# Optimization experiments

Measured on AMD Instinct MI355X. Metric: run time of the kernel, lower is better.

The kernel has to match this reference:

```python
import jax, jax.numpy as jnp
import numpy as np

MIN_SIZE = 16.0
PH, PW, SCALE = 7, 7, 0.0625


def _context_anchor(rois, hh, hw):
    """rois: [N,5] (batch_idx,x1,y1,x2,y2). Returns [N*8,5] context boxes, col0 = 0 label."""
    N = rois.shape[0]
    x1, y1, x2, y2 = rois[:, 1], rois[:, 2], rois[:, 3], rois[:, 4]
    w, h = x2 - x1, y2 - y1
    k = jnp.arange(3, dtype=rois.dtype)
    sx = x1[:, None] + w[:, None] * (k - 0.5)  # x1 - w + w*k + w/2
    sy = y1[:, None] + h[:, None] * (k - 0.5)
    # np.meshgrid(shift_x, shift_y).ravel() is y-major
    cx = jnp.broadcast_to(sx[:, None, :], (N, 3, 3)).reshape(N, 9)
    cy = jnp.broadcast_to(sy[:, :, None], (N, 3, 3)).reshape(N, 9)
    boxes = jnp.stack([cx - w[:, None] / 4, cy - h[:, None] / 4,
                       cx + w[:, None] / 4, cy + h[:, None] / 4], -1)  # [N,9,4]
    bw = boxes[..., 2] - boxes[..., 0] + 1
    bh = boxes[..., 3] - boxes[..., 1] + 1
    invalid = ((boxes[..., 0] < 0) | (boxes[..., 1] < 0) |
               (boxes[..., 2] >= hw) | (boxes[..., 3] >= hh) |
               (bw < MIN_SIZE) | (bh < MIN_SIZE))
    boxes = jnp.where(invalid[..., None], rois[:, None, 1:5], boxes)
    boxes = boxes[:, jnp.array([0, 1, 2, 3, 5, 6, 7, 8]), :]  # drop center cell
    gt = boxes.reshape(N * 8, 4)  # K = 8N
    # IoU(all roi boxes, gt) with +1 pixel convention (bbox_overlaps_batch)
    A = rois[:, 1:5]
    aw, ah = A[:, 2] - A[:, 0] + 1, A[:, 3] - A[:, 1] + 1
    gw, gh = gt[:, 2] - gt[:, 0] + 1, gt[:, 3] - gt[:, 1] + 1
    iw = jnp.maximum(jnp.minimum(A[:, None, 2], gt[None, :, 2]) - jnp.maximum(A[:, None, 0], gt[None, :, 0]) + 1, 0)
    ih = jnp.maximum(jnp.minimum(A[:, None, 3], gt[None, :, 3]) - jnp.maximum(A[:, None, 1], gt[None, :, 1]) + 1, 0)
    inter = iw * ih
    ov = inter / ((aw * ah)[:, None] + (gw * gh)[None, :] - inter)  # [N,K]
    ov = jnp.where(((gw == 1) & (gh == 1))[None, :], 0.0, ov)
    ov = jnp.where(((aw == 1) & (ah == 1))[:, None], -1.0, ov)
    gt_max = ov.max(0)          # best overlap per gt box
    best = ov.argmax(0)         # index of best-matching roi (torch's `_`)
    labels = gt_max >= 0.3
    w_cell, h_cell = gt[:, 2] - gt[:, 0], gt[:, 3] - gt[:, 1]
    rw = jnp.where(labels, rois[best, 3] - rois[best, 1], 0.0)
    rh = jnp.where(labels, rois[best, 4] - rois[best, 2], 0.0)
    labels = (labels & ~(jnp.maximum(rw, rh) >= jnp.maximum(w_cell, h_cell))
                     & ~(jnp.minimum(rw, rh) < jnp.minimum(w_cell, h_cell) / 3))
    gt = jnp.where(labels[:, None], rois[best][:, 1:5], gt)
    # original zeroes labels at the end -> label column is all zeros
    return jnp.concatenate([jnp.zeros((N * 8, 1), rois.dtype), gt], -1)


def _roi_pool(features, boxes, ph, pw, scale):
    """Classic Caffe max RoIPool. Assumes batch_size==1 (all batch indices 0)."""
    _, C, H, W = features.shape
    f = features[0]  # [C,H,W]
    sw = jnp.round(boxes[:, 1] * scale)
    sh = jnp.round(boxes[:, 2] * scale)
    ew = jnp.round(boxes[:, 3] * scale)
    eh = jnp.round(boxes[:, 4] * scale)
    bsh = jnp.maximum(eh - sh + 1, 1.0) / ph
    bsw = jnp.maximum(ew - sw + 1, 1.0) / pw
    ii = jnp.arange(ph, dtype=f.dtype)
    jj = jnp.arange(pw, dtype=f.dtype)
    hs = jnp.clip(jnp.floor(ii[None, :] * bsh[:, None]) + sh[:, None], 0, H)   # [R,ph]
    he = jnp.clip(jnp.ceil((ii[None, :] + 1) * bsh[:, None]) + sh[:, None], 0, H)
    ws = jnp.clip(jnp.floor(jj[None, :] * bsw[:, None]) + sw[:, None], 0, W)   # [R,pw]
    we = jnp.clip(jnp.ceil((jj[None, :] + 1) * bsw[:, None]) + sw[:, None], 0, W)
    hidx = jnp.arange(H, dtype=f.dtype)
    widx = jnp.arange(W, dtype=f.dtype)
    mask_h = (hidx >= hs[..., None]) & (hidx < he[..., None])  # [R,ph,H]
    mask_w = (widx >= ws[..., None]) & (widx < we[..., None])  # [R,pw,W]
    NEG = jnp.asarray(-1e30, f.dtype)
    # separable masked max: reduce W per pw-bin, then H per ph-bin
    colmax = jnp.stack([jnp.where(mask_w[:, j, None, None, :], f[None], NEG).max(-1)
                        for j in range(pw)], axis=1)           # [R,pw,C,H]
    out = jnp.stack([jnp.where(mask_h[:, i, None, None, :], colmax, NEG).max(-1)
                     for i in range(ph)], axis=1)              # [R,ph,pw,C]
    valid = mask_h.any(-1)[:, :, None] & mask_w.any(-1)[:, None, :]
    out = jnp.where(valid[..., None], out, 0.0)                # empty bins -> 0
    return jnp.transpose(out, (0, 3, 1, 2))                    # [R,C,ph,pw]


def reference(features, rois, hh, hw):
    N = rois.shape[0]
    gt = _context_anchor(rois, hh, hw).reshape(N, 8, 5)
    cat_rois = jnp.concatenate([rois[:, None, :], gt], 1).reshape(-1, 5)  # [9N,5]
    pool = _roi_pool(features, cat_rois, PH, PW, SCALE)                   # [9N,C,7,7]
    pool_feat = pool.reshape(N, -1, PW, PH)                               # [N,9C,7,7]
    return pool_feat, cat_rois


def setup_inputs() -> dict:
    key = jax.random.key(0)
    k1, k2, k3, k4, k5 = jax.random.split(key, 5)
    N, C, Hf, Wf, IMG = 32, 256, 40, 40, 640
    x1 = jax.random.uniform(k1, (N,), minval=0.0, maxval=IMG - 220.0)
    y1 = jax.random.uniform(k2, (N,), minval=0.0, maxval=IMG - 220.0)
    bw = jax.random.uniform(k3, (N,), minval=80.0, maxval=200.0)
    bh = jax.random.uniform(k4, (N,), minval=80.0, maxval=200.0)
    rois = jnp.stack([jnp.zeros((N,)), x1, y1, x1 + bw, y1 + bh], -1).astype(jnp.float32)
    features = jax.random.normal(k5, (1, C, Hf, Wf), dtype=jnp.float32)
    return {"features": features, "rois": rois, "hh": 640, "hw": 640}
```

## Files before the change

kernel.cpp:

```cpp
#include <hip/hip_runtime.h>
#include <math.h>

#define N_ROIS   32
#define N_GT     (N_ROIS * 8)
#define N_CAT    (N_ROIS * 9)
#define C_FEAT   256
#define H_FEAT   40
#define W_FEAT   40
#define P_FEAT   (H_FEAT * W_FEAT)
#define PH       7
#define PW       7
#define SCALE    0.0625f
#define MIN_SIZE 16.0f
#define CELLS    (PH * PW)
#define POOL_PER_BOX (C_FEAT * CELLS)
#define OUT_POOL_ELEMS ((size_t)N_CAT * POOL_PER_BOX)

#define N_TRANS_BLOCKS (P_FEAT / 32 * (C_FEAT / 32))
#define WIN 16

__global__ void prep_kernel(const float* __restrict__ f,
                            const float* __restrict__ rois,
                            const int* __restrict__ hh_p,
                            const int* __restrict__ hw_p,
                            float* __restrict__ ft,
                            float* __restrict__ cat_out,
                            int use_transpose) {
    __shared__ float tile[32][33];
    __shared__ float R[N_ROIS * 5];
    const int bid = blockIdx.x;
    const int tid = threadIdx.x;

    if (bid < N_TRANS_BLOCKS) {
        if (!use_transpose) return;
        const int pt = (bid % (P_FEAT / 32)) * 32;
        const int ct = (bid / (P_FEAT / 32)) * 32;
        const int lx = tid & 31;
        const int ly = tid >> 5;
        #pragma unroll
        for (int i = 0; i < 32; i += 8)
            tile[ly + i][lx] = f[(ct + ly + i) * P_FEAT + (pt + lx)];
        __syncthreads();
        #pragma unroll
        for (int i = 0; i < 32; i += 8)
            ft[(pt + ly + i) * C_FEAT + (ct + lx)] = tile[lx][ly + i];
        return;
    }

    if (tid < N_ROIS * 5) R[tid] = rois[tid];
    __syncthreads();

    const float hh = (float)(*hh_p);
    const float hw = (float)(*hw_p);

    const int g = tid;
    const int n = g >> 3;
    const int j = g & 7;
    const int m = (j < 4) ? j : j + 1;
    const int r  = m / 3;
    const int cc = m % 3;

    const float x1 = R[n * 5 + 1], y1 = R[n * 5 + 2];
    const float x2 = R[n * 5 + 3], y2 = R[n * 5 + 4];
    const float w = x2 - x1, h = y2 - y1;

    const float cx = x1 + w * ((float)cc - 0.5f);
    const float cy = y1 + h * ((float)r  - 0.5f);
    float bx1 = cx - w * 0.25f;
    float by1 = cy - h * 0.25f;
    float bx2 = cx + w * 0.25f;
    float by2 = cy + h * 0.25f;
    const float bw = bx2 - bx1 + 1.0f;
    const float bh = by2 - by1 + 1.0f;
    const bool invalid = (bx1 < 0.0f) || (by1 < 0.0f) ||
                         (bx2 >= hw) || (by2 >= hh) ||
                         (bw < MIN_SIZE) || (bh < MIN_SIZE);
    if (invalid) { bx1 = x1; by1 = y1; bx2 = x2; by2 = y2; }

    const float gw = bx2 - bx1 + 1.0f;
    const float gh = by2 - by1 + 1.0f;
    const float garea = gw * gh;
    const bool gdeg = (gw == 1.0f) && (gh == 1.0f);

    float best_ov = -INFINITY;
    int best = 0;
    for (int a = 0; a < N_ROIS; ++a) {
        const float ax1 = R[a * 5 + 1], ay1 = R[a * 5 + 2];
        const float ax2 = R[a * 5 + 3], ay2 = R[a * 5 + 4];
        const float aw = ax2 - ax1 + 1.0f, ah = ay2 - ay1 + 1.0f;
        float iw = fminf(ax2, bx2) - fmaxf(ax1, bx1) + 1.0f;
        float ih = fminf(ay2, by2) - fmaxf(ay1, by1) + 1.0f;
        iw = fmaxf(iw, 0.0f);
        ih = fmaxf(ih, 0.0f);
        const float inter = iw * ih;
        float ov = inter / (aw * ah + garea - inter);
        if (gdeg) ov = 0.0f;
        if (aw == 1.0f && ah == 1.0f) ov = -1.0f;
        if (ov > best_ov) { best_ov = ov; best = a; }
    }

    bool label = (best_ov >= 0.3f);
    const float w_cell = bx2 - bx1;
    const float h_cell = by2 - by1;
    const float rw = label ? (R[best * 5 + 3] - R[best * 5 + 1]) : 0.0f;
    const float rh = label ? (R[best * 5 + 4] - R[best * 5 + 2]) : 0.0f;
    label = label &&
            !(fmaxf(rw, rh) >= fmaxf(w_cell, h_cell)) &&
            !(fminf(rw, rh) < fminf(w_cell, h_cell) / 3.0f);
    if (label) {
        bx1 = R[best * 5 + 1]; by1 = R[best * 5 + 2];
        bx2 = R[best * 5 + 3]; by2 = R[best * 5 + 4];
    }

    float* row = cat_out + (size_t)(n * 9 + 1 + j) * 5;
    row[0] = 0.0f;
    row[1] = bx1; row[2] = by1; row[3] = bx2; row[4] = by2;
    if (j == 0) {
        float* rr = cat_out + (size_t)(n * 9) * 5;
        #pragma unroll
        for (int t = 0; t < 5; ++t) rr[t] = R[n * 5 + t];
    }
}

__global__ __launch_bounds__(256) void
roi_pool_kernel(const float* __restrict__ feat,
                const float* __restrict__ cat_rois,
                float* __restrict__ out) {
    const int b = blockIdx.x / PH;
    const int i = blockIdx.x % PH;
    const int c = threadIdx.x;

    const float* cr = cat_rois + (size_t)b * 5;
    const float x1 = cr[1], y1 = cr[2], x2 = cr[3], y2 = cr[4];
    const float sw = rintf(x1 * SCALE);
    const float sh = rintf(y1 * SCALE);
    const float ew = rintf(x2 * SCALE);
    const float eh = rintf(y2 * SCALE);
    const float bsh = fmaxf(eh - sh + 1.0f, 1.0f) * (1.0f / (float)PH);
    const float bsw = fmaxf(ew - sw + 1.0f, 1.0f) * (1.0f / (float)PW);

    int hs = (int)fminf(fmaxf(floorf((float)i * bsh) + sh, 0.0f), (float)H_FEAT);
    int he = (int)fminf(fmaxf(ceilf((float)(i + 1) * bsh) + sh, 0.0f), (float)H_FEAT);

    int ws[PW], we[PW];
    #pragma unroll
    for (int j = 0; j < PW; ++j) {
        ws[j] = (int)fminf(fmaxf(floorf((float)j * bsw) + sw, 0.0f), (float)W_FEAT);
        we[j] = (int)fminf(fmaxf(ceilf((float)(j + 1) * bsw) + sw, 0.0f), (float)W_FEAT);
    }

    hs = __builtin_amdgcn_readfirstlane(hs);
    he = __builtin_amdgcn_readfirstlane(he);
    #pragma unroll
    for (int j = 0; j < PW; ++j) {
        ws[j] = __builtin_amdgcn_readfirstlane(ws[j]);
        we[j] = __builtin_amdgcn_readfirstlane(we[j]);
    }
    const int xs = ws[0];
    const bool wide = (we[PW - 1] > xs + WIN);

    float mx[PW];
    #pragma unroll
    for (int j = 0; j < PW; ++j) mx[j] = -1e30f;

    for (int y = hs; y < he; ++y) {
        const float* fr = feat + (size_t)(y * W_FEAT) * C_FEAT + c;
        float win[WIN];
        #pragma unroll
        for (int k = 0; k < WIN; ++k) {
            int x = xs + k;
            x = (x < W_FEAT - 1) ? x : (W_FEAT - 1);
            win[k] = fr[(size_t)x * C_FEAT];
        }
        #pragma unroll
        for (int j = 0; j < PW; ++j) {
            #pragma unroll
            for (int k = 0; k < WIN; ++k) {
                const int x = xs + k;
                if (x >= ws[j] && x < we[j])
                    mx[j] = fmaxf(mx[j], win[k]);
            }
        }
        if (wide) {
            #pragma unroll
            for (int j = 0; j < PW; ++j) {
                int x0 = (ws[j] > xs + WIN) ? ws[j] : (xs + WIN);
                for (int x = x0; x < we[j]; ++x)
                    mx[j] = fmaxf(mx[j], fr[(size_t)x * C_FEAT]);
            }
        }
    }

    const bool rowv = (he > hs);
    float* ob = out + (size_t)b * POOL_PER_BOX + (size_t)c * CELLS + i * PW;
    #pragma unroll
    for (int j = 0; j < PW; ++j)
        ob[j] = (rowv && (we[j] > ws[j])) ? mx[j] : 0.0f;
}

__global__ __launch_bounds__(256) void
roi_pool_kernel_nchw(const float* __restrict__ feat,
                     const float* __restrict__ cat_rois,
                     float* __restrict__ out) {
    const int b = blockIdx.x / PH;
    const int i = blockIdx.x % PH;
    const int c = threadIdx.x;

    const float* cr = cat_rois + (size_t)b * 5;
    const float sw = rintf(cr[1] * SCALE);
    const float sh = rintf(cr[2] * SCALE);
    const float ew = rintf(cr[3] * SCALE);
    const float eh = rintf(cr[4] * SCALE);
    const float bsh = fmaxf(eh - sh + 1.0f, 1.0f) * (1.0f / (float)PH);
    const float bsw = fmaxf(ew - sw + 1.0f, 1.0f) * (1.0f / (float)PW);

    const int hs = (int)fminf(fmaxf(floorf((float)i * bsh) + sh, 0.0f), (float)H_FEAT);
    const int he = (int)fminf(fmaxf(ceilf((float)(i + 1) * bsh) + sh, 0.0f), (float)H_FEAT);
    int ws[PW], we[PW];
    #pragma unroll
    for (int j = 0; j < PW; ++j) {
        ws[j] = (int)fminf(fmaxf(floorf((float)j * bsw) + sw, 0.0f), (float)W_FEAT);
        we[j] = (int)fminf(fmaxf(ceilf((float)(j + 1) * bsw) + sw, 0.0f), (float)W_FEAT);
    }
    float mx[PW];
    #pragma unroll
    for (int j = 0; j < PW; ++j) mx[j] = -1e30f;
    for (int y = hs; y < he; ++y) {
        const float* fr = feat + (size_t)c * P_FEAT + y * W_FEAT;
        #pragma unroll
        for (int j = 0; j < PW; ++j)
            for (int x = ws[j]; x < we[j]; ++x)
                mx[j] = fmaxf(mx[j], fr[x]);
    }
    const bool rowv = (he > hs);
    float* ob = out + (size_t)b * POOL_PER_BOX + (size_t)c * CELLS + i * PW;
    #pragma unroll
    for (int j = 0; j < PW; ++j)
        ob[j] = (rowv && (we[j] > ws[j])) ? mx[j] : 0.0f;
}

extern "C" void kernel_launch(void* const* d_in, const int* in_sizes, int n_in,
                              void* d_out, int out_size, void* d_ws, size_t ws_size,
                              hipStream_t stream) {
    const float* features = (const float*)d_in[0];
    const float* rois     = (const float*)d_in[1];
    const int*   hh_p     = (const int*)d_in[2];
    const int*   hw_p     = (const int*)d_in[3];

    float* out      = (float*)d_out;
    float* cat_out  = out + OUT_POOL_ELEMS;
    float* ft       = (float*)d_ws;

    const size_t ft_bytes = (size_t)C_FEAT * P_FEAT * sizeof(float);
    const int use_transpose = (ws_size >= ft_bytes) ? 1 : 0;

    hipLaunchKernelGGL(prep_kernel, dim3(N_TRANS_BLOCKS + 1), dim3(256), 0, stream,
                       features, rois, hh_p, hw_p, ft, cat_out, use_transpose);

    if (use_transpose) {
        hipLaunchKernelGGL(roi_pool_kernel, dim3(N_CAT * PH), dim3(C_FEAT), 0, stream,
                           ft, cat_out, out);
    } else {
        hipLaunchKernelGGL(roi_pool_kernel_nchw, dim3(N_CAT * PH), dim3(C_FEAT), 0, stream,
                           features, cat_out, out);
    }
}
```

Measured before the change: 92.90 us.

## Remap ROI pool block order and add narrow-bin triangular window path

The block index mapping is swapped so consecutive blocks handle different boxes for the same bin row instead of the 7 rows of one box, which changes cache locality and scheduling. The pooling loop is split into a narrow path (bin width at most 2, with a 14-wide register window and a triangular per-bin bound plus branchless selects) and a generic direct-loop path for wider bins. The readfirstlane scalarization of the bin bounds is removed, which may push bound arithmetic into vector registers. The triangular bound relies on bins starting within 2*j of xs, which holds only for narrow bins.

```diff
diff --git a/kernel.cpp b/kernel.cpp
--- a/kernel.cpp
+++ b/kernel.cpp
@@ -2,7 +2,6 @@
 #include <math.h>
 
 #define N_ROIS   32
-#define N_GT     (N_ROIS * 8)
 #define N_CAT    (N_ROIS * 9)
 #define C_FEAT   256
 #define H_FEAT   40
@@ -17,7 +16,7 @@
 #define OUT_POOL_ELEMS ((size_t)N_CAT * POOL_PER_BOX)
 
 #define N_TRANS_BLOCKS (P_FEAT / 32 * (C_FEAT / 32))
-#define WIN 16
+#define WIN 14
 
 __global__ void prep_kernel(const float* __restrict__ f,
                             const float* __restrict__ rois,
@@ -126,8 +125,8 @@
 roi_pool_kernel(const float* __restrict__ feat,
                 const float* __restrict__ cat_rois,
                 float* __restrict__ out) {
-    const int b = blockIdx.x / PH;
-    const int i = blockIdx.x % PH;
+    const int i = blockIdx.x / N_CAT;
+    const int b = blockIdx.x % N_CAT;
     const int c = threadIdx.x;
 
     const float* cr = cat_rois + (size_t)b * 5;
@@ -139,8 +138,8 @@
     const float bsh = fmaxf(eh - sh + 1.0f, 1.0f) * (1.0f / (float)PH);
     const float bsw = fmaxf(ew - sw + 1.0f, 1.0f) * (1.0f / (float)PW);
 
-    int hs = (int)fminf(fmaxf(floorf((float)i * bsh) + sh, 0.0f), (float)H_FEAT);
-    int he = (int)fminf(fmaxf(ceilf((float)(i + 1) * bsh) + sh, 0.0f), (float)H_FEAT);
+    const int hs = (int)fminf(fmaxf(floorf((float)i * bsh) + sh, 0.0f), (float)H_FEAT);
+    const int he = (int)fminf(fmaxf(ceilf((float)(i + 1) * bsh) + sh, 0.0f), (float)H_FEAT);
 
     int ws[PW], we[PW];
     #pragma unroll
@@ -149,45 +148,43 @@
         we[j] = (int)fminf(fmaxf(ceilf((float)(j + 1) * bsw) + sw, 0.0f), (float)W_FEAT);
     }
 
-    hs = __builtin_amdgcn_readfirstlane(hs);
-    he = __builtin_amdgcn_readfirstlane(he);
-    #pragma unroll
-    for (int j = 0; j < PW; ++j) {
-        ws[j] = __builtin_amdgcn_readfirstlane(ws[j]);
-        we[j] = __builtin_amdgcn_readfirstlane(we[j]);
-    }
     const int xs = ws[0];
-    const bool wide = (we[PW - 1] > xs + WIN);
+    const bool narrow = (bsw <= 2.0f);
 
     float mx[PW];
     #pragma unroll
     for (int j = 0; j < PW; ++j) mx[j] = -1e30f;
 
-    for (int y = hs; y < he; ++y) {
-        const float* fr = feat + (size_t)(y * W_FEAT) * C_FEAT + c;
-        float win[WIN];
-        #pragma unroll
-        for (int k = 0; k < WIN; ++k) {
-            int x = xs + k;
-            x = (x < W_FEAT - 1) ? x : (W_FEAT - 1);
-            win[k] = fr[(size_t)x * C_FEAT];
-        }
-        #pragma unroll
-        for (int j = 0; j < PW; ++j) {
+    if (narrow) {
+        for (int y = hs; y < he; ++y) {
+            const float* fr = feat + (size_t)(y * W_FEAT) * C_FEAT + c;
+            float win[WIN];
             #pragma unroll
             for (int k = 0; k < WIN; ++k) {
-                const int x = xs + k;
-                if (x >= ws[j] && x < we[j])
-                    mx[j] = fmaxf(mx[j], win[k]);
+                int x = xs + k;
+                x = (x < W_FEAT - 1) ? x : (W_FEAT - 1);
+                win[k] = fr[(size_t)x * C_FEAT];
+            }
+            #pragma unroll
+            for (int j = 0; j < PW; ++j) {
+                const int lo = ws[j], hi = we[j];
+                const int kmax = (2 * j + 2 < WIN) ? (2 * j + 2) : WIN;
+                #pragma unroll
+                for (int k = 0; k < kmax; ++k) {
+                    const int x = xs + k;
+                    const bool in = (x >= lo) & (x < hi);
+                    const float t = fmaxf(mx[j], win[k]);
+                    mx[j] = in ? t : mx[j];
+                }
             }
         }
-        if (wide) {
+    } else {
+        for (int y = hs; y < he; ++y) {
+            const float* fr = feat + (size_t)(y * W_FEAT) * C_FEAT + c;
             #pragma unroll
-            for (int j = 0; j < PW; ++j) {
-                int x0 = (ws[j] > xs + WIN) ? ws[j] : (xs + WIN);
-                for (int x = x0; x < we[j]; ++x)
+            for (int j = 0; j < PW; ++j)
+                for (int x = ws[j]; x < we[j]; ++x)
                     mx[j] = fmaxf(mx[j], fr[(size_t)x * C_FEAT]);
-            }
         }
     }
 
@@ -202,8 +199,8 @@
 roi_pool_kernel_nchw(const float* __restrict__ feat,
                      const float* __restrict__ cat_rois,
                      float* __restrict__ out) {
-    const int b = blockIdx.x / PH;
-    const int i = blockIdx.x % PH;
+    const int i = blockIdx.x / N_CAT;
+    const int b = blockIdx.x % N_CAT;
     const int c = threadIdx.x;
 
     const float* cr = cat_rois + (size_t)b * 5;
@@ -258,10 +255,10 @@
                        features, rois, hh_p, hw_p, ft, cat_out, use_transpose);
 
     if (use_transpose) {
-        hipLaunchKernelGGL(roi_pool_kernel, dim3(N_CAT * PH), dim3(C_FEAT), 0, stream,
+        hipLaunchKernelGGL(roi_pool_kernel, dim3(PH * N_CAT), dim3(C_FEAT), 0, stream,
                            ft, cat_out, out);
     } else {
-        hipLaunchKernelGGL(roi_pool_kernel_nchw, dim3(N_CAT * PH), dim3(C_FEAT), 0, stream,
+        hipLaunchKernelGGL(roi_pool_kernel_nchw, dim3(PH * N_CAT), dim3(C_FEAT), 0, stream,
                            features, cat_out, out);
     }
 }
```

Result: faster. 82.42 us (-11.3%).
